# Optimization experiments

Hardware: AMD Instinct MI355X
Metric: run time of the kernel (lower is better)

## Reference

```python
import jax, jax.numpy as jnp
import numpy as np

XYZ_MIN, XYZ_MAX = -1.0, 1.0
GRID = 160                                   # world_size per axis
VOXEL_SIZE = (XYZ_MAX - XYZ_MIN) / GRID      # 0.0125
ALPHA_INIT = 0.01
ACT_SHIFT = float(np.log(1.0 / (1.0 - ALPHA_INIT) - 1.0))
NEAR, FAR = 0.2, 6.0
STEPSIZE = 0.5
INTERVAL = STEPSIZE * 1.0                    # voxel_size_ratio == 1
N_SAMPLES = int(np.linalg.norm(np.array([GRID + 1] * 3)) / STEPSIZE) + 1  # 558
BG = 1.0


def trilinear_sample(grid, xyz):
    """grid: [C,X,Y,Z]; xyz: [...,3] world coords. F.grid_sample bilinear, align_corners=True."""
    size = np.array(grid.shape[1:])
    u = (xyz - XYZ_MIN) / (XYZ_MAX - XYZ_MIN)          # [...,3] in [0,1] (inside bbox)
    idx = u * (size - 1).astype(np.float32)            # align_corners=True index space
    i0 = jnp.floor(idx).astype(jnp.int32)
    frac = idx - i0
    lo = jnp.clip(i0, 0, size - 1)
    hi = jnp.clip(i0 + 1, 0, size - 1)
    out = 0.0
    for bx in (0, 1):
        for by in (0, 1):
            for bz in (0, 1):
                ix = hi[..., 0] if bx else lo[..., 0]
                iy = hi[..., 1] if by else lo[..., 1]
                iz = hi[..., 2] if bz else lo[..., 2]
                w = ((frac[..., 0] if bx else 1.0 - frac[..., 0]) *
                     (frac[..., 1] if by else 1.0 - frac[..., 1]) *
                     (frac[..., 2] if bz else 1.0 - frac[..., 2]))
                out = out + grid[:, ix, iy, iz] * w[None]
    return jnp.moveaxis(out, 0, -1)                    # [...,C]


def setup_inputs() -> dict:
    key = jax.random.key(0)
    k1, k2, k3, k4 = jax.random.split(key, 4)
    N = 16384
    o = jax.random.normal(k1, (N, 3), dtype=jnp.float32)
    rays_o = o / jnp.linalg.norm(o, axis=-1, keepdims=True) * 3.0   # on sphere r=3, outside bbox
    d = -rays_o + 0.3 * jax.random.normal(k2, (N, 3), dtype=jnp.float32)
    rays_d = d / jnp.linalg.norm(d, axis=-1, keepdims=True)         # point toward origin
    density = jax.random.normal(k3, (1, 1, GRID, GRID, GRID), dtype=jnp.float32)
    k0 = 0.5 * jax.random.normal(k4, (1, 3, GRID, GRID, GRID), dtype=jnp.float32)
    return {"rays_o": rays_o, "rays_d": rays_d, "density": density, "k0": k0}


def reference(rays_o, rays_d, density, k0):
    # --- sample_ray (is_train=False) ---
    vec = jnp.where(rays_d == 0, jnp.float32(1e-6), rays_d)
    rate_a = (XYZ_MAX - rays_o) / vec
    rate_b = (XYZ_MIN - rays_o) / vec
    t_min = jnp.clip(jnp.minimum(rate_a, rate_b).max(-1), NEAR, FAR)   # [N]
    t_max = jnp.clip(jnp.maximum(rate_a, rate_b).min(-1), NEAR, FAR)
    ray_oob = t_max < t_min                                            # ray misses bbox
    rng = jnp.arange(N_SAMPLES, dtype=rays_o.dtype)                    # [S]
    step = STEPSIZE * VOXEL_SIZE * rng
    interpx = t_min[:, None] + step[None, :] / jnp.linalg.norm(rays_d, axis=-1, keepdims=True)  # [N,S]
    rays_pts = rays_o[:, None, :] + rays_d[:, None, :] * interpx[..., None]                     # [N,S,3]
    mask_oob = ray_oob[:, None] | ((rays_pts < XYZ_MIN) | (rays_pts > XYZ_MAX)).any(-1)         # [N,S]

    # --- density -> alpha (activate_density), zero outside bbox ---
    dens = trilinear_sample(density[0], rays_pts)[..., 0]              # [N,S]
    alpha = jnp.where(mask_oob, 0.0,
                      1.0 - jnp.exp(-jax.nn.softplus(dens + ACT_SHIFT) * INTERVAL))

    # --- alpha compositing ---
    ones = jnp.ones_like(alpha[:, :1])
    alphainv_cum = jnp.concatenate([ones, jnp.cumprod(1.0 - alpha, axis=-1)], axis=-1)  # [N,S+1]
    weights = alpha * alphainv_cum[:, :-1]                             # [N,S]

    # --- color (rgbnet is None -> sigmoid of k0) and ray marching ---
    rgb = jax.nn.sigmoid(trilinear_sample(k0[0], rays_pts))            # [N,S,3]
    rgb_marched = jnp.einsum('ns,nsc->nc', weights, rgb) + alphainv_cum[:, -1:] * BG
    return rgb_marched
```

## Files before the change

kernel.cpp:

```cpp
#include <hip/hip_runtime.h>
#include <math.h>

#define G 160
#define GM1 159
#define NS 558
#define CHSTRIDE (160 * 160 * 160)
#define G3 (160 * 160 * 160)

#define DENS_SCALE (10.0f / 255.0f)
#define DENS_BIAS  (-5.0f)
#define COL_SCALE  (7.0f / 255.0f)
#define COL_BIAS   (-3.5f)

#define NBUCKET 512
#define MAXRAYS 16384


__device__ __forceinline__ unsigned int q8(float v, float bias, float invscale) {
    return (unsigned int)lrintf(fminf(fmaxf((v - bias) * invscale, 0.f), 255.f));
}

__global__ __launch_bounds__(1024) void prep_fused(
    const float* __restrict__ dens,
    const float* __restrict__ k0,
    const float* __restrict__ rays_o,
    const float* __restrict__ rays_d,
    unsigned int* __restrict__ packed,
    unsigned int* __restrict__ order, int N)
{
    __shared__ unsigned short skeys[MAXRAYS];
    __shared__ unsigned int hist[NBUCKET];
    __shared__ unsigned int tmp[NBUCKET];
    __shared__ unsigned int offs[NBUCKET];

    const int tid = threadIdx.x;

    if (blockIdx.x == 0) {
        for (int i = tid; i < NBUCKET; i += 1024) hist[i] = 0;
        __syncthreads();
        for (int r = tid; r < N; r += 1024) {
            const float ox = rays_o[r * 3 + 0], oy = rays_o[r * 3 + 1], oz = rays_o[r * 3 + 2];
            const float dx = rays_d[r * 3 + 0], dy = rays_d[r * 3 + 1], dz = rays_d[r * 3 + 2];
            const float vx = (dx == 0.f) ? 1e-6f : dx;
            const float vy = (dy == 0.f) ? 1e-6f : dy;
            const float vz = (dz == 0.f) ? 1e-6f : dz;
            const float rax = (1.f - ox) / vx, rbx = (-1.f - ox) / vx;
            const float ray_ = (1.f - oy) / vy, rby = (-1.f - oy) / vy;
            const float raz = (1.f - oz) / vz, rbz = (-1.f - oz) / vz;
            float tmin = fmaxf(fmaxf(fminf(rax, rbx), fminf(ray_, rby)), fminf(raz, rbz));
            tmin = fminf(fmaxf(tmin, 0.2f), 6.0f);
            const float px = fminf(fmaxf(fmaf(dx, tmin, ox), -1.f), 1.f);
            const float py = fminf(fmaxf(fmaf(dy, tmin, oy), -1.f), 1.f);
            const float pz = fminf(fmaxf(fmaf(dz, tmin, oz), -1.f), 1.f);
            const int cx = min(7, (int)((px + 1.f) * 4.f));
            const int cy = min(7, (int)((py + 1.f) * 4.f));
            const int cz = min(7, (int)((pz + 1.f) * 4.f));
            const unsigned int key = (unsigned int)((cx << 6) | (cy << 3) | cz);
            skeys[r] = (unsigned short)key;
            atomicAdd(&hist[key], 1u);
        }
        __syncthreads();
        if (tid < NBUCKET) tmp[tid] = hist[tid];
        __syncthreads();
        for (int off = 1; off < NBUCKET; off <<= 1) {
            unsigned int v = 0;
            if (tid < NBUCKET && tid >= off) v = tmp[tid - off];
            __syncthreads();
            if (tid < NBUCKET) tmp[tid] += v;
            __syncthreads();
        }
        if (tid < NBUCKET) offs[tid] = tmp[tid] - hist[tid];
        __syncthreads();
        for (int r = tid; r < N; r += 1024) {
            const unsigned int pos = atomicAdd(&offs[skeys[r]], 1u);
            order[pos] = (unsigned int)r;
        }
    } else {
        const int base = ((blockIdx.x - 1) * 1024 + tid) * 4;
        if (base + 3 < G3) {
            const float4 d = *(const float4*)(dens + base);
            const float4 r = *(const float4*)(k0 + base);
            const float4 g = *(const float4*)(k0 + CHSTRIDE + base);
            const float4 b = *(const float4*)(k0 + 2 * CHSTRIDE + base);
            const float dis = 255.f / 10.f, cis = 255.f / 7.f;
            uint4 o;
            o.x = q8(d.x, DENS_BIAS, dis) | (q8(r.x, COL_BIAS, cis) << 8) |
                  (q8(g.x, COL_BIAS, cis) << 16) | (q8(b.x, COL_BIAS, cis) << 24);
            o.y = q8(d.y, DENS_BIAS, dis) | (q8(r.y, COL_BIAS, cis) << 8) |
                  (q8(g.y, COL_BIAS, cis) << 16) | (q8(b.y, COL_BIAS, cis) << 24);
            o.z = q8(d.z, DENS_BIAS, dis) | (q8(r.z, COL_BIAS, cis) << 8) |
                  (q8(g.z, COL_BIAS, cis) << 16) | (q8(b.z, COL_BIAS, cis) << 24);
            o.w = q8(d.w, DENS_BIAS, dis) | (q8(r.w, COL_BIAS, cis) << 8) |
                  (q8(g.w, COL_BIAS, cis) << 16) | (q8(b.w, COL_BIAS, cis) << 24);
            *(uint4*)(packed + base) = o;
        }
    }
}


__device__ __forceinline__ float ub(unsigned int q, int c) {
    return (float)((q >> (c * 8)) & 0xffu);
}

struct SampleData {
    unsigned int q000, q001, q010, q011, q100, q101, q110, q111;
    float w000, w001, w010, w011, w100, w101, w110, w111;
    float amask;
};

__device__ __forceinline__ SampleData fetch_sample(
    const unsigned int* __restrict__ pg,
    float ex, float ey, float ez, float gx, float gy, float gz, int s)
{
    SampleData r;
    const float sF = (float)s;
    const float fx = fmaf(gx, sF, ex);
    const float fy = fmaf(gy, sF, ey);
    const float fz = fmaf(gz, sF, ez);
    const bool valid = (fx >= 0.f) && (fx <= 159.f) && (fy >= 0.f) &&
                       (fy <= 159.f) && (fz >= 0.f) && (fz <= 159.f);
    r.amask = valid ? 1.f : 0.f;
    const float cfx = __builtin_amdgcn_fmed3f(fx, 0.f, 159.f);
    const float cfy = __builtin_amdgcn_fmed3f(fy, 0.f, 159.f);
    const float cfz = __builtin_amdgcn_fmed3f(fz, 0.f, 159.f);
    const int x0 = (int)cfx; const float tx = cfx - (float)x0;
    const int y0 = (int)cfy; const float ty = cfy - (float)y0;
    const int z0 = (int)cfz; const float tz = cfz - (float)z0;
    const int x1 = min(x0 + 1, GM1);
    const int y1 = min(y0 + 1, GM1);
    const float mx = 1.f - tx, my = 1.f - ty, mz = 1.f - tz;
    const float w00 = mx * my, w01 = mx * ty, w10 = tx * my, w11 = tx * ty;
    r.w000 = w00 * mz; r.w001 = w00 * tz;
    r.w010 = w01 * mz; r.w011 = w01 * tz;
    r.w100 = w10 * mz; r.w101 = w10 * tz;
    r.w110 = w11 * mz; r.w111 = w11 * tz;
    const int xg0 = x0 * G, xg1 = x1 * G;
    const int i00 = (xg0 + y0) * G + z0;
    const int i01 = (xg0 + y1) * G + z0;
    const int i10 = (xg1 + y0) * G + z0;
    const int i11 = (xg1 + y1) * G + z0;
    r.q000 = pg[i00]; r.q001 = pg[i00 + 1];
    r.q010 = pg[i01]; r.q011 = pg[i01 + 1];
    r.q100 = pg[i10]; r.q101 = pg[i10 + 1];
    r.q110 = pg[i11]; r.q111 = pg[i11 + 1];
    return r;
}

__device__ __forceinline__ void shade(const SampleData& d,
    float& alpha, float& cr, float& cg, float& cb)
{
    const float ACT_SHIFT = -4.59511985013459f;
    float acc[4];
    #pragma unroll
    for (int ch = 0; ch < 4; ++ch) {
        acc[ch] = d.w000 * ub(d.q000, ch) + d.w001 * ub(d.q001, ch) +
                  d.w010 * ub(d.q010, ch) + d.w011 * ub(d.q011, ch) +
                  d.w100 * ub(d.q100, ch) + d.w101 * ub(d.q101, ch) +
                  d.w110 * ub(d.q110, ch) + d.w111 * ub(d.q111, ch);
    }
    const float dens = fmaf(acc[0], DENS_SCALE, DENS_BIAS);
    const float vr   = fmaf(acc[1], COL_SCALE,  COL_BIAS);
    const float vg   = fmaf(acc[2], COL_SCALE,  COL_BIAS);
    const float vb   = fmaf(acc[3], COL_SCALE,  COL_BIAS);
    const float e = __expf(dens + ACT_SHIFT);
    alpha = (1.f - __builtin_amdgcn_rsqf(1.f + e)) * d.amask;
    cr = __builtin_amdgcn_rcpf(1.f + __expf(-vr));
    cg = __builtin_amdgcn_rcpf(1.f + __expf(-vg));
    cb = __builtin_amdgcn_rcpf(1.f + __expf(-vb));
}

__global__ __launch_bounds__(256) void dvgo_render_u8(
    const float* __restrict__ rays_o,
    const float* __restrict__ rays_d,
    const unsigned int* __restrict__ pg,
    const unsigned int* __restrict__ order,
    float* __restrict__ out, int N)
{
    unsigned int bid = blockIdx.x;
    const unsigned int nblk = gridDim.x;
    if ((nblk & 511u) == 0u) {
        const unsigned int xcd  = bid & 7u;
        const unsigned int step = bid >> 3;
        const unsigned int cseq = step >> 6;
        const unsigned int pos  = step & 63u;
        bid = (cseq * 8u + xcd) * 64u + pos;
    } else if ((nblk & 7u) == 0u) {
        bid = (bid & 7u) * (nblk >> 3) + (bid >> 3);
    }
    const int slot = (int)(bid * 4 + (threadIdx.x >> 6));
    const int lane = (int)(threadIdx.x & 63u);
    if (slot >= N) return;
    const int wave = order ? (int)order[slot] : slot;

    const float ox = rays_o[wave * 3 + 0], oy = rays_o[wave * 3 + 1], oz = rays_o[wave * 3 + 2];
    const float dx = rays_d[wave * 3 + 0], dy = rays_d[wave * 3 + 1], dz = rays_d[wave * 3 + 2];
    const float inv_norm = __builtin_amdgcn_rsqf(dx * dx + dy * dy + dz * dz);

    const float vx = (dx == 0.f) ? 1e-6f : dx;
    const float vy = (dy == 0.f) ? 1e-6f : dy;
    const float vz = (dz == 0.f) ? 1e-6f : dz;
    const float rax = (1.f - ox) / vx, rbx = (-1.f - ox) / vx;
    const float ray_ = (1.f - oy) / vy, rby = (-1.f - oy) / vy;
    const float raz = (1.f - oz) / vz, rbz = (-1.f - oz) / vz;
    float tmin = fmaxf(fmaxf(fminf(rax, rbx), fminf(ray_, rby)), fminf(raz, rbz));
    float tmax = fminf(fminf(fmaxf(rax, rbx), fmaxf(ray_, rby)), fmaxf(raz, rbz));
    tmin = fminf(fmaxf(tmin, 0.2f), 6.0f);
    tmax = fminf(fmaxf(tmax, 0.2f), 6.0f);

    const float dt = 0.00625f * inv_norm;

    const float ex = (fmaf(dx, tmin, ox) + 1.f) * 79.5f;
    const float ey = (fmaf(dy, tmin, oy) + 1.f) * 79.5f;
    const float ez = (fmaf(dz, tmin, oz) + 1.f) * 79.5f;
    const float gx = dx * dt * 79.5f;
    const float gy = dy * dt * 79.5f;
    const float gz = dz * dt * 79.5f;

    int n_samp = 0;
    if (!(tmax < tmin)) n_samp = min(NS, (int)((tmax - tmin) / dt) + 2);
    const int n_chunks = (n_samp + 63) >> 6;

    float T = 1.f;
    float ar = 0.f, ag = 0.f, ab = 0.f;

    if (n_chunks > 0) {
        SampleData sd0 = fetch_sample(pg, ex, ey, ez, gx, gy, gz, lane);
        SampleData sd1;
        if (n_chunks > 1) sd1 = fetch_sample(pg, ex, ey, ez, gx, gy, gz, 64 + lane);
        for (int c = 0; c < n_chunks; ++c) {
            SampleData sd2;
            if (c + 2 < n_chunks)
                sd2 = fetch_sample(pg, ex, ey, ez, gx, gy, gz, ((c + 2) << 6) + lane);

            float alpha, cr, cg, cb;
            shade(sd0, alpha, cr, cg, cb);

            float incl = 1.f - alpha;
            #pragma unroll
            for (int off = 1; off < 64; off <<= 1) {
                const float v = __shfl_up(incl, off, 64);
                if (lane >= off) incl *= v;
            }
            float excl = __shfl_up(incl, 1, 64);
            if (lane == 0) excl = 1.f;

            const float w = alpha * T * excl;
            ar = fmaf(w, cr, ar);
            ag = fmaf(w, cg, ag);
            ab = fmaf(w, cb, ab);
            T *= __shfl(incl, 63, 64);

            sd0 = sd1;
            sd1 = sd2;
        }
    }

    #pragma unroll
    for (int off = 32; off > 0; off >>= 1) {
        ar += __shfl_down(ar, off, 64);
        ag += __shfl_down(ag, off, 64);
        ab += __shfl_down(ab, off, 64);
    }
    if (lane == 0) {
        out[wave * 3 + 0] = ar + T;
        out[wave * 3 + 1] = ag + T;
        out[wave * 3 + 2] = ab + T;
    }
}


__global__ __launch_bounds__(256) void dvgo_render_f32(
    const float* __restrict__ rays_o,
    const float* __restrict__ rays_d,
    const float* __restrict__ dens_g,
    const float* __restrict__ k0_g,
    float* __restrict__ out, int N)
{
    const int wave = (int)((blockIdx.x * 256u + threadIdx.x) >> 6);
    const int lane = (int)(threadIdx.x & 63u);
    if (wave >= N) return;

    const float ox = rays_o[wave * 3 + 0], oy = rays_o[wave * 3 + 1], oz = rays_o[wave * 3 + 2];
    const float dx = rays_d[wave * 3 + 0], dy = rays_d[wave * 3 + 1], dz = rays_d[wave * 3 + 2];
    const float inv_norm = rsqrtf(dx * dx + dy * dy + dz * dz);

    const float vx = (dx == 0.f) ? 1e-6f : dx;
    const float vy = (dy == 0.f) ? 1e-6f : dy;
    const float vz = (dz == 0.f) ? 1e-6f : dz;
    const float rax = (1.f - ox) / vx, rbx = (-1.f - ox) / vx;
    const float ray_ = (1.f - oy) / vy, rby = (-1.f - oy) / vy;
    const float raz = (1.f - oz) / vz, rbz = (-1.f - oz) / vz;
    float tmin = fmaxf(fmaxf(fminf(rax, rbx), fminf(ray_, rby)), fminf(raz, rbz));
    float tmax = fminf(fminf(fmaxf(rax, rbx), fmaxf(ray_, rby)), fmaxf(raz, rbz));
    tmin = fminf(fmaxf(tmin, 0.2f), 6.0f);
    tmax = fminf(fmaxf(tmax, 0.2f), 6.0f);
    const bool ray_oob = (tmax < tmin);

    const float dt = 0.00625f * inv_norm;
    const float ACT_SHIFT = -4.59511985013459f;

    float T = 1.f;
    float ar = 0.f, ag = 0.f, ab = 0.f;

    for (int s0 = 0; s0 < NS; s0 += 64) {
        const int s = s0 + lane;
        float alpha = 0.f, cr = 0.f, cg = 0.f, cb = 0.f;
        bool valid = false;
        if (!ray_oob && s < NS) {
            const float t = tmin + dt * (float)s;
            const float px = fmaf(dx, t, ox);
            const float py = fmaf(dy, t, oy);
            const float pz = fmaf(dz, t, oz);
            if (px >= -1.f && px <= 1.f && py >= -1.f && py <= 1.f &&
                pz >= -1.f && pz <= 1.f) {
                valid = true;
                const float fx = (px + 1.f) * 79.5f;
                const float fy = (py + 1.f) * 79.5f;
                const float fz = (pz + 1.f) * 79.5f;
                int x0 = (int)fx; const float tx = fx - (float)x0;
                int y0 = (int)fy; const float ty = fy - (float)y0;
                int z0 = (int)fz; const float tz = fz - (float)z0;
                x0 = min(x0, GM1); y0 = min(y0, GM1); z0 = min(z0, GM1);
                const int x1 = min(x0 + 1, GM1);
                const int y1 = min(y0 + 1, GM1);
                const int z1 = min(z0 + 1, GM1);

                const float mx = 1.f - tx, my = 1.f - ty, mz = 1.f - tz;
                const float w00 = mx * my, w01 = mx * ty, w10 = tx * my, w11 = tx * ty;
                const float w000 = w00 * mz, w001 = w00 * tz;
                const float w010 = w01 * mz, w011 = w01 * tz;
                const float w100 = w10 * mz, w101 = w10 * tz;
                const float w110 = w11 * mz, w111 = w11 * tz;

                const int b00 = (x0 * G + y0) * G;
                const int b01 = (x0 * G + y1) * G;
                const int b10 = (x1 * G + y0) * G;
                const int b11 = (x1 * G + y1) * G;

                const float dens =
                    w000 * dens_g[b00 + z0] + w001 * dens_g[b00 + z1] +
                    w010 * dens_g[b01 + z0] + w011 * dens_g[b01 + z1] +
                    w100 * dens_g[b10 + z0] + w101 * dens_g[b10 + z1] +
                    w110 * dens_g[b11 + z0] + w111 * dens_g[b11 + z1];

                const float e = __expf(dens + ACT_SHIFT);
                alpha = 1.f - rsqrtf(1.f + e);

                #pragma unroll
                for (int ch = 0; ch < 3; ++ch) {
                    const float* k0c = k0_g + ch * CHSTRIDE;
                    const float v =
                        w000 * k0c[b00 + z0] + w001 * k0c[b00 + z1] +
                        w010 * k0c[b01 + z0] + w011 * k0c[b01 + z1] +
                        w100 * k0c[b10 + z0] + w101 * k0c[b10 + z1] +
                        w110 * k0c[b11 + z0] + w111 * k0c[b11 + z1];
                    const float sg = 1.f / (1.f + __expf(-v));
                    if (ch == 0) cr = sg; else if (ch == 1) cg = sg; else cb = sg;
                }
            }
        }

        float incl = 1.f - alpha;
        #pragma unroll
        for (int off = 1; off < 64; off <<= 1) {
            const float v = __shfl_up(incl, off, 64);
            if (lane >= off) incl *= v;
        }
        float excl = __shfl_up(incl, 1, 64);
        if (lane == 0) excl = 1.f;

        const float w = alpha * T * excl;
        ar = fmaf(w, cr, ar);
        ag = fmaf(w, cg, ag);
        ab = fmaf(w, cb, ab);

        T *= __shfl(incl, 63, 64);

        if (__ballot(valid) == 0ull) break;
        if (T < 1e-5f) break;
    }

    #pragma unroll
    for (int off = 32; off > 0; off >>= 1) {
        ar += __shfl_down(ar, off, 64);
        ag += __shfl_down(ag, off, 64);
        ab += __shfl_down(ab, off, 64);
    }
    if (lane == 0) {
        out[wave * 3 + 0] = ar + T;
        out[wave * 3 + 1] = ag + T;
        out[wave * 3 + 2] = ab + T;
    }
}

extern "C" void kernel_launch(void* const* d_in, const int* in_sizes, int n_in,
                              void* d_out, int out_size, void* d_ws, size_t ws_size,
                              hipStream_t stream) {
    const float* rays_o  = (const float*)d_in[0];
    const float* rays_d  = (const float*)d_in[1];
    const float* density = (const float*)d_in[2];
    const float* k0      = (const float*)d_in[3];
    float* out = (float*)d_out;
    const int N = in_sizes[0] / 3;

    const int blocks = (N * 64 + 255) / 256;

    const size_t grid_b  = (size_t)G3 * 4;
    const size_t need = grid_b + (size_t)N * 4;

    if (ws_size >= need && N <= MAXRAYS) {
        unsigned int* packed = (unsigned int*)d_ws;
        unsigned int* order  = (unsigned int*)((char*)d_ws + grid_b);
        const int pack_blocks = (G3 + 4095) / 4096;
        prep_fused<<<pack_blocks + 1, 1024, 0, stream>>>(density, k0, rays_o, rays_d,
                                                         packed, order, N);
        dvgo_render_u8<<<blocks, 256, 0, stream>>>(rays_o, rays_d, packed, order, out, N);
    } else {
        dvgo_render_f32<<<blocks, 256, 0, stream>>>(rays_o, rays_d, density, k0, out, N);
    }
}
```

Before: 87.45 us.

## Rotate triple-buffered sample fetches and fuse shading with compositing

The chunk loop is unrolled by three so the prefetched sample buffers rotate in place instead of being copied each iteration. Shading and the wave-wide transmittance scan are merged into one composite routine. The exclusive product is now the inclusive product divided by (1-alpha), which replaces a shuffle. The bounds mask uses min/max reductions, and launch bounds request 6 waves per SIMD. In exchange, fetches are issued unconditionally past the last chunk (clamped, so wasted bandwidth). Dividing by (1-alpha) loses precision when alpha nears 1.

```diff
diff --git a/kernel.cpp b/kernel.cpp
--- a/kernel.cpp
+++ b/kernel.cpp
@@ -117,9 +117,9 @@
     const float fx = fmaf(gx, sF, ex);
     const float fy = fmaf(gy, sF, ey);
     const float fz = fmaf(gz, sF, ez);
-    const bool valid = (fx >= 0.f) && (fx <= 159.f) && (fy >= 0.f) &&
-                       (fy <= 159.f) && (fz >= 0.f) && (fz <= 159.f);
-    r.amask = valid ? 1.f : 0.f;
+    const float mn = fminf(fminf(fx, fy), fz);
+    const float mx_ = fmaxf(fmaxf(fx, fy), fz);
+    r.amask = (mn >= 0.f && mx_ <= 159.f) ? 1.f : 0.f;
     const float cfx = __builtin_amdgcn_fmed3f(fx, 0.f, 159.f);
     const float cfy = __builtin_amdgcn_fmed3f(fy, 0.f, 159.f);
     const float cfz = __builtin_amdgcn_fmed3f(fz, 0.f, 159.f);
@@ -146,8 +146,8 @@
     return r;
 }
 
-__device__ __forceinline__ void shade(const SampleData& d,
-    float& alpha, float& cr, float& cg, float& cb)
+__device__ __forceinline__ void composite(const SampleData& d, int lane,
+    float& T, float& ar, float& ag, float& ab)
 {
     const float ACT_SHIFT = -4.59511985013459f;
     float acc[4];
@@ -163,13 +163,28 @@
     const float vg   = fmaf(acc[2], COL_SCALE,  COL_BIAS);
     const float vb   = fmaf(acc[3], COL_SCALE,  COL_BIAS);
     const float e = __expf(dens + ACT_SHIFT);
-    alpha = (1.f - __builtin_amdgcn_rsqf(1.f + e)) * d.amask;
-    cr = __builtin_amdgcn_rcpf(1.f + __expf(-vr));
-    cg = __builtin_amdgcn_rcpf(1.f + __expf(-vg));
-    cb = __builtin_amdgcn_rcpf(1.f + __expf(-vb));
-}
-
-__global__ __launch_bounds__(256) void dvgo_render_u8(
+    const float oma = __builtin_amdgcn_rsqf(1.f + e);
+    const float alpha = (1.f - oma) * d.amask;
+    const float cr = __builtin_amdgcn_rcpf(1.f + __expf(-vr));
+    const float cg = __builtin_amdgcn_rcpf(1.f + __expf(-vg));
+    const float cb = __builtin_amdgcn_rcpf(1.f + __expf(-vb));
+
+    const float one_m_a = 1.f - alpha;
+    float incl = one_m_a;
+    #pragma unroll
+    for (int off = 1; off < 64; off <<= 1) {
+        const float v = __shfl_up(incl, off, 64);
+        if (lane >= off) incl *= v;
+    }
+    const float excl = incl * __builtin_amdgcn_rcpf(one_m_a);
+    const float w = alpha * T * excl;
+    ar = fmaf(w, cr, ar);
+    ag = fmaf(w, cg, ag);
+    ab = fmaf(w, cb, ab);
+    T *= __shfl(incl, 63, 64);
+}
+
+__global__ __launch_bounds__(256, 6) void dvgo_render_u8(
     const float* __restrict__ rays_o,
     const float* __restrict__ rays_d,
     const unsigned int* __restrict__ pg,
@@ -218,41 +233,27 @@
 
     int n_samp = 0;
     if (!(tmax < tmin)) n_samp = min(NS, (int)((tmax - tmin) / dt) + 2);
-    const int n_chunks = (n_samp + 63) >> 6;
+    const int nc = (n_samp + 63) >> 6;
 
     float T = 1.f;
     float ar = 0.f, ag = 0.f, ab = 0.f;
 
-    if (n_chunks > 0) {
-        SampleData sd0 = fetch_sample(pg, ex, ey, ez, gx, gy, gz, lane);
-        SampleData sd1;
-        if (n_chunks > 1) sd1 = fetch_sample(pg, ex, ey, ez, gx, gy, gz, 64 + lane);
-        for (int c = 0; c < n_chunks; ++c) {
-            SampleData sd2;
-            if (c + 2 < n_chunks)
-                sd2 = fetch_sample(pg, ex, ey, ez, gx, gy, gz, ((c + 2) << 6) + lane);
-
-            float alpha, cr, cg, cb;
-            shade(sd0, alpha, cr, cg, cb);
-
-            float incl = 1.f - alpha;
-            #pragma unroll
-            for (int off = 1; off < 64; off <<= 1) {
-                const float v = __shfl_up(incl, off, 64);
-                if (lane >= off) incl *= v;
-            }
-            float excl = __shfl_up(incl, 1, 64);
-            if (lane == 0) excl = 1.f;
-
-            const float w = alpha * T * excl;
-            ar = fmaf(w, cr, ar);
-            ag = fmaf(w, cg, ag);
-            ab = fmaf(w, cb, ab);
-            T *= __shfl(incl, 63, 64);
-
-            sd0 = sd1;
-            sd1 = sd2;
-        }
+    if (nc > 0) {
+        SampleData A = fetch_sample(pg, ex, ey, ez, gx, gy, gz, lane);
+        SampleData B = fetch_sample(pg, ex, ey, ez, gx, gy, gz, 64 + lane);
+        SampleData C;
+        int c = 0;
+        while (c + 3 <= nc) {
+            C = fetch_sample(pg, ex, ey, ez, gx, gy, gz, ((c + 2) << 6) + lane);
+            composite(A, lane, T, ar, ag, ab);
+            A = fetch_sample(pg, ex, ey, ez, gx, gy, gz, ((c + 3) << 6) + lane);
+            composite(B, lane, T, ar, ag, ab);
+            B = fetch_sample(pg, ex, ey, ez, gx, gy, gz, ((c + 4) << 6) + lane);
+            composite(C, lane, T, ar, ag, ab);
+            c += 3;
+        }
+        if (c < nc) composite(A, lane, T, ar, ag, ab);
+        if (c + 1 < nc) composite(B, lane, T, ar, ag, ab);
     }
 
     #pragma unroll
```

Result: slower. 124.1 us (+41.9%).
